# Kernel optimization log

Measured on AMD Instinct MI355X. Metric: run time of the kernel, lower is better.

Reference implementation:

```python
import jax, jax.numpy as jnp
import numpy as np

H_DIM = 64
GRID = 8
NBR = 2.0
BN_EPS = 1e-5
N_SEQ = 64
N_PED = 64
BOTTLENECK = 1024


def setup_inputs() -> dict:
    key = jax.random.key(0)
    k0, k1, k2, k3 = jax.random.split(key, 4)
    batch = N_SEQ * N_PED
    h_states = jax.random.normal(k0, (1, batch, H_DIM), jnp.float32)
    # positions spread over a 4x4 area so some neighbors fall inside the 2.0 neighborhood
    end_pos = jax.random.uniform(k1, (batch, 2), jnp.float32) * 4.0
    rel_pos = jax.random.normal(k2, (batch, 2), jnp.float32)
    starts = jnp.arange(N_SEQ, dtype=jnp.int32) * N_PED
    seq_start_end = jnp.stack([starts, starts + N_PED], axis=1)
    in_dim = GRID * GRID * H_DIM  # 4096
    W = jax.random.normal(k3, (in_dim, BOTTLENECK), jnp.float32) / np.sqrt(in_dim)
    b = jnp.zeros((BOTTLENECK,), jnp.float32)
    gamma = jnp.ones((BOTTLENECK,), jnp.float32)
    beta = jnp.zeros((BOTTLENECK,), jnp.float32)
    return {"h_states": h_states, "seq_start_end": seq_start_end, "end_pos": end_pos,
            "rel_pos": rel_pos, "W": W, "b": b, "gamma": gamma, "beta": beta}


def _pool_scene(hidden, pos):
    # hidden: (n, h), pos: (n, 2). Pair (i, j): ped j binned into ped i's grid.
    n, h = hidden.shape
    g2 = GRID * GRID
    half = NBR / 2.0
    tl_x = pos[:, 0] - half
    tl_y = pos[:, 1] + half
    br_x = pos[:, 0] + half
    br_y = pos[:, 1] - half
    px = pos[None, :, 0]  # (1, n) -> broadcast over i
    py = pos[None, :, 1]
    cell_x = jnp.floor((px - tl_x[:, None]) / NBR * GRID)
    cell_y = jnp.floor((tl_y[:, None] - py) / NBR * GRID)
    grid = (cell_x + cell_y * GRID).astype(jnp.int32) + 1  # slot 0 = trash bin
    oob = ((px >= br_x[:, None]) | (px <= tl_x[:, None]) |
           (py >= tl_y[:, None]) | (py <= br_y[:, None]) |
           jnp.eye(n, dtype=bool))  # self-interaction excluded
    grid = grid + (jnp.arange(n, dtype=jnp.int32) * g2)[:, None]
    grid = jnp.where(oob, 0, grid)  # (n, n)
    src = jnp.broadcast_to(hidden[None], (n, n, h)).reshape(-1, h)
    buf = jnp.zeros((n * g2 + 1, h), hidden.dtype).at[grid.reshape(-1)].add(src)
    return buf[1:].reshape(n, g2 * h)


def reference(h_states, seq_start_end, end_pos, rel_pos, W, b, gamma, beta):
    batch = end_pos.shape[0]
    n_seq = seq_start_end.shape[0]
    n_ped = batch // n_seq  # equal-length scenes by construction
    hid = h_states.reshape(-1, H_DIM).reshape(n_seq, n_ped, H_DIM)
    pos = end_pos.reshape(n_seq, n_ped, 2)
    pool_h = jax.vmap(_pool_scene)(hid, pos).reshape(batch, -1)  # (batch, 4096)
    x = pool_h @ W + b
    # BatchNorm1d in training mode (batch statistics, biased variance)
    mean = jnp.mean(x, axis=0)
    var = jnp.var(x, axis=0)
    x = (x - mean) * jax.lax.rsqrt(var + BN_EPS) * gamma + beta
    return jax.nn.relu(x)
```

## Files before the change

### kernel.cpp

```cpp
#include <hip/hip_runtime.h>
#include <hip/hip_bf16.h>


#define NPED  64
#define BATCH 4096
#define HDIM  64
#define G2    64
#define KDIM  4096
#define NOUT  1024

typedef __attribute__((ext_vector_type(8))) short short8;
typedef __attribute__((ext_vector_type(4))) float f32x4;

__device__ __forceinline__ unsigned short f2bf(float f) {
    __hip_bfloat16 h = __float2bfloat16(f);
    return *reinterpret_cast<unsigned short*>(&h);
}

__device__ __forceinline__ void lds_load16(const void* g, void* l) {
    __builtin_amdgcn_global_load_lds(
        (const __attribute__((address_space(1))) void*)g,
        (__attribute__((address_space(3))) void*)l, 16, 0, 0);
}

__global__ __launch_bounds__(256) void pool_kernel(const float* __restrict__ h,
                                                   const float* __restrict__ pos,
                                                   unsigned short* __restrict__ A2) {
    __shared__ float acc[4][G2 * HDIM];
    __shared__ float pl[NPED * 2];
    int t = threadIdx.x;
    int w = t >> 6, lane = t & 63;
    int p0 = blockIdx.x * 4;
    int sbase = p0 & ~(NPED - 1);
    if (t < 128) pl[t] = pos[sbase * 2 + t];
    #pragma unroll
    for (int c = 0; c < G2; ++c) acc[w][c * HDIM + lane] = 0.f;
    __syncthreads();

    int i = p0 + w;
    int il = i & (NPED - 1);
    float cx0 = pl[2 * il], cy0 = pl[2 * il + 1];
    float tlx = cx0 - 1.f, tly = cy0 + 1.f, brx = cx0 + 1.f, bry = cy0 - 1.f;
    for (int jb = 0; jb < NPED; jb += 8) {
        float hv[8];
        #pragma unroll
        for (int u = 0; u < 8; ++u)
            hv[u] = h[(size_t)(sbase + jb + u) * HDIM + lane];
        #pragma unroll
        for (int u = 0; u < 8; ++u) {
            int j = jb + u;
            float px = pl[2 * j], py = pl[2 * j + 1];
            if (j != il && !(px >= brx || px <= tlx || py >= tly || py <= bry)) {
                int cellx = (int)floorf((px - tlx) * 4.f);
                int celly = (int)floorf((tly - py) * 4.f);
                int cell = cellx + celly * 8;
                if ((unsigned)cell < 64u)
                    atomicAdd(&acc[w][cell * HDIM + lane], hv[u]);
            }
        }
    }
    __syncthreads();

    int mtile = p0 >> 4, r0 = p0 & 15;
    unsigned int* out = (unsigned int*)A2 + (size_t)mtile * 32768 + r0 * 4;
    #pragma unroll
    for (int p = 0; p < 32; ++p) {
        int lin = p * 256 + t;
        int fragidx = lin >> 4;
        int rr = (lin >> 2) & 3, q = lin & 3;
        int k = fragidx * 8 + q * 2;
        unsigned int v = (unsigned int)f2bf(acc[rr][k]) |
                         ((unsigned int)f2bf(acc[rr][k + 1]) << 16);
        out[fragidx * 64 + rr * 4 + q] = v;
    }
}

__global__ __launch_bounds__(256) void wt_kernel(const float* __restrict__ W,
                                                 unsigned short* __restrict__ Wt,
                                                 float* __restrict__ stats) {
    __shared__ unsigned short tile[64][66];
    int k0 = blockIdx.x * 64;
    int n0 = blockIdx.y * 64;
    int t = threadIdx.x;
    if (blockIdx.x == 0 && blockIdx.y < 8) stats[blockIdx.y * 256 + t] = 0.f;
    #pragma unroll
    for (int p = 0; p < 4; ++p) {
        int lin = p * 256 + t;
        int c4 = lin & 15, kl = lin >> 4;
        float4 v = ((const float4*)(W + (size_t)(k0 + kl) * NOUT + n0))[c4];
        tile[c4 * 4 + 0][kl] = f2bf(v.x);
        tile[c4 * 4 + 1][kl] = f2bf(v.y);
        tile[c4 * 4 + 2][kl] = f2bf(v.z);
        tile[c4 * 4 + 3][kl] = f2bf(v.w);
    }
    __syncthreads();
    unsigned int* out = (unsigned int*)Wt;
    #pragma unroll
    for (int p = 0; p < 8; ++p) {
        int lin = p * 256 + t;
        int ku = lin & 31, nl = lin >> 5;
        unsigned int v = (unsigned int)tile[nl][2 * ku] |
                         ((unsigned int)tile[nl][2 * ku + 1] << 16);
        out[(size_t)(n0 + nl) * (KDIM / 2) + (k0 >> 1) + ku] = v;
    }
}

__global__ __launch_bounds__(256, 2) void gemm_kernel(const unsigned short* __restrict__ A2,
                                                      const unsigned short* __restrict__ Bt,
                                                      float* __restrict__ C,
                                                      float* __restrict__ P1,
                                                      float* __restrict__ P2,
                                                      float* __restrict__ P3) {
    __shared__ __align__(16) unsigned short Bs[128 * 64];
    int t = threadIdx.x;
    int w = t >> 6, lane = t & 63;
    int m0 = blockIdx.x * 256, n0 = blockIdx.y * 128;
    int kbase = blockIdx.z * 1024;
    int wm = w * 64;

    f32x4 acc[4][8];
    #pragma unroll
    for (int i = 0; i < 4; ++i)
        #pragma unroll
        for (int j = 0; j < 8; ++j)
            acc[i][j] = (f32x4){0.f, 0.f, 0.f, 0.f};

    int rbase = w * 32 + (lane >> 3);
    int koff = ((lane & 7) ^ (lane >> 3)) * 8;
    const unsigned short* Bg = Bt + (size_t)(n0 + rbase) * KDIM + kbase + koff;
    unsigned short* BsW = Bs + w * 2048 + lane * 8;

    const unsigned short* Abase = A2 + (size_t)((m0 + wm) >> 4) * 65536 + lane * 8;
    int ktile0 = kbase >> 5;

    for (int kt = 0; kt < 1024; kt += 64) {
        #pragma unroll
        for (int q = 0; q < 4; ++q)
            lds_load16(Bg + (size_t)q * 8 * KDIM + kt, BsW + q * 512);
        short8 af[2][4];
        int ktile = ktile0 + (kt >> 5);
        #pragma unroll
        for (int kk = 0; kk < 2; ++kk)
            #pragma unroll
            for (int i = 0; i < 4; ++i)
                af[kk][i] = *(const short8*)(Abase + ((size_t)i * 128 + ktile + kk) * 512);
        __syncthreads();
        #pragma unroll
        for (int kk = 0; kk < 2; ++kk) {
            int chunk = ((kk * 4 + (lane >> 4)) ^ (lane & 7)) * 8;
            #pragma unroll
            for (int j = 0; j < 8; ++j) {
                short8 b = *(const short8*)&Bs[(j * 16 + (lane & 15)) * 64 + chunk];
                #pragma unroll
                for (int i = 0; i < 4; ++i)
                    acc[i][j] = __builtin_amdgcn_mfma_f32_16x16x32_bf16(af[kk][i], b, acc[i][j], 0, 0, 0);
            }
        }
        __syncthreads();
    }

    float* dst = blockIdx.z == 0 ? C : blockIdx.z == 1 ? P1 : blockIdx.z == 2 ? P2 : P3;
    int col0 = n0 + (lane & 15);
    int row0 = m0 + wm + ((lane >> 4) << 2);
    #pragma unroll
    for (int i = 0; i < 4; ++i)
        #pragma unroll
        for (int j = 0; j < 8; ++j)
            #pragma unroll
            for (int r = 0; r < 4; ++r)
                dst[(size_t)(row0 + i * 16 + r) * NOUT + col0 + j * 16] = acc[i][j][r];
}

__global__ __launch_bounds__(256) void combine_stats(float* __restrict__ C,
                                                     const float* __restrict__ P1,
                                                     const float* __restrict__ P2,
                                                     const float* __restrict__ P3,
                                                     float* __restrict__ stats) {
    int t = threadIdx.x;
    int colchunk = blockIdx.x & 3;
    int rowchunk = blockIdx.x >> 2;
    int col = colchunk * 256 + t;
    size_t base = (size_t)rowchunk * 32 * NOUT + col;
    float s = 0.f, s2 = 0.f;
    #pragma unroll 4
    for (int r = 0; r < 32; ++r) {
        size_t ix = base + (size_t)r * NOUT;
        float v = (C[ix] + P1[ix]) + (P2[ix] + P3[ix]);
        C[ix] = v;
        s += v; s2 += v * v;
    }
    atomicAdd(&stats[col], s);
    atomicAdd(&stats[NOUT + col], s2);
}

__global__ __launch_bounds__(256) void norm_kernel(float* __restrict__ C,
                                                   const float* __restrict__ stats,
                                                   const float* __restrict__ gamma,
                                                   const float* __restrict__ beta) {
    int idx = blockIdx.x * 256 + threadIdx.x;
    int col4 = idx & 255;
    float4 x = ((const float4*)C)[idx];
    float4 s = ((const float4*)stats)[col4];
    float4 q = ((const float4*)(stats + NOUT))[col4];
    float4 g = ((const float4*)gamma)[col4];
    float4 b = ((const float4*)beta)[col4];
    const float inv_n = 1.f / 4096.f;
    float m, inv;
    m = s.x * inv_n; inv = rsqrtf(q.x * inv_n - m * m + 1e-5f); x.x = fmaxf((x.x - m) * inv * g.x + b.x, 0.f);
    m = s.y * inv_n; inv = rsqrtf(q.y * inv_n - m * m + 1e-5f); x.y = fmaxf((x.y - m) * inv * g.y + b.y, 0.f);
    m = s.z * inv_n; inv = rsqrtf(q.z * inv_n - m * m + 1e-5f); x.z = fmaxf((x.z - m) * inv * g.z + b.z, 0.f);
    m = s.w * inv_n; inv = rsqrtf(q.w * inv_n - m * m + 1e-5f); x.w = fmaxf((x.w - m) * inv * g.w + b.w, 0.f);
    ((float4*)C)[idx] = x;
}

extern "C" void kernel_launch(void* const* d_in, const int* in_sizes, int n_in,
                              void* d_out, int out_size, void* d_ws, size_t ws_size,
                              hipStream_t stream) {
    const float* h      = (const float*)d_in[0];
    const float* endpos = (const float*)d_in[2];
    const float* W      = (const float*)d_in[4];
    const float* gamma  = (const float*)d_in[6];
    const float* beta   = (const float*)d_in[7];
    float* C = (float*)d_out;

    char* ws = (char*)d_ws;
    size_t off = 0;
    unsigned short* A2 = (unsigned short*)(ws + off); off += (size_t)BATCH * KDIM * 2;
    unsigned short* Wt = (unsigned short*)(ws + off); off += (size_t)NOUT * KDIM * 2;
    float* P1 = (float*)(ws + off); off += (size_t)BATCH * NOUT * 4;
    float* P2 = (float*)(ws + off); off += (size_t)BATCH * NOUT * 4;
    float* P3 = (float*)(ws + off); off += (size_t)BATCH * NOUT * 4;
    float* stats = (float*)(ws + off);

    pool_kernel<<<BATCH / 4, 256, 0, stream>>>(h, endpos, A2);
    wt_kernel<<<dim3(KDIM / 64, NOUT / 64), 256, 0, stream>>>(W, Wt, stats);
    gemm_kernel<<<dim3(BATCH / 256, NOUT / 128, 4), 256, 0, stream>>>(A2, Wt, C, P1, P2, P3);
    combine_stats<<<512, 256, 0, stream>>>(C, P1, P2, P3, stats);
    norm_kernel<<<(BATCH * NOUT / 4) / 256, 256, 0, stream>>>(C, stats, gamma, beta);
}
```

Measured before the change: 174.6 us.

## Replace LDS atomic scatter pooling with ballot-based per-cell gather

The pooling kernel drops the per-wave LDS accumulator and its atomicAdd scatter. Each lane now bins one neighbour, and for each of the 64 cells a wavefront ballot yields the mask of contributing neighbours. Every lane then sums those neighbours' hidden values for its own feature from a scene hidden tile staged in LDS, and writes bf16 straight to the swizzled A layout. Blocks grow to 8 pedestrians and 512 threads. This removes the atomics, the zeroing pass and the second sync, at the cost of 64 ballots per wave and strided 2-byte global stores.

```diff
diff --git a/kernel.cpp b/kernel.cpp
--- a/kernel.cpp
+++ b/kernel.cpp
@@ -23,55 +23,49 @@
         (__attribute__((address_space(3))) void*)l, 16, 0, 0);
 }
 
-__global__ __launch_bounds__(256) void pool_kernel(const float* __restrict__ h,
+__global__ __launch_bounds__(512) void pool_kernel(const float* __restrict__ h,
                                                    const float* __restrict__ pos,
                                                    unsigned short* __restrict__ A2) {
-    __shared__ float acc[4][G2 * HDIM];
+    __shared__ float hs[NPED * HDIM];
     __shared__ float pl[NPED * 2];
     int t = threadIdx.x;
     int w = t >> 6, lane = t & 63;
-    int p0 = blockIdx.x * 4;
+    int p0 = blockIdx.x * 8;
     int sbase = p0 & ~(NPED - 1);
     if (t < 128) pl[t] = pos[sbase * 2 + t];
-    #pragma unroll
-    for (int c = 0; c < G2; ++c) acc[w][c * HDIM + lane] = 0.f;
+    {
+        const float4* src = (const float4*)(h + (size_t)sbase * HDIM);
+        float4* dst = (float4*)hs;
+        dst[t] = src[t];
+        dst[t + 512] = src[t + 512];
+    }
     __syncthreads();
 
     int i = p0 + w;
     int il = i & (NPED - 1);
     float cx0 = pl[2 * il], cy0 = pl[2 * il + 1];
     float tlx = cx0 - 1.f, tly = cy0 + 1.f, brx = cx0 + 1.f, bry = cy0 - 1.f;
-    for (int jb = 0; jb < NPED; jb += 8) {
-        float hv[8];
-        #pragma unroll
-        for (int u = 0; u < 8; ++u)
-            hv[u] = h[(size_t)(sbase + jb + u) * HDIM + lane];
-        #pragma unroll
-        for (int u = 0; u < 8; ++u) {
-            int j = jb + u;
-            float px = pl[2 * j], py = pl[2 * j + 1];
-            if (j != il && !(px >= brx || px <= tlx || py >= tly || py <= bry)) {
-                int cellx = (int)floorf((px - tlx) * 4.f);
-                int celly = (int)floorf((tly - py) * 4.f);
-                int cell = cellx + celly * 8;
-                if ((unsigned)cell < 64u)
-                    atomicAdd(&acc[w][cell * HDIM + lane], hv[u]);
-            }
+    float px = pl[2 * lane], py = pl[2 * lane + 1];
+    bool inb = (lane != il) && !(px >= brx || px <= tlx || py >= tly || py <= bry);
+    int cellx = (int)floorf((px - tlx) * 4.f);
+    int celly = (int)floorf((tly - py) * 4.f);
+    int cell = cellx + celly * 8;
+    inb = inb && ((unsigned)cell < 64u);
+
+    int mtile = i >> 4, r = i & 15;
+    unsigned short* outb = A2 + (size_t)mtile * 65536 + r * 8
+                              + (lane >> 5) * 512 + ((lane >> 3) & 3) * 128 + (lane & 7);
+    const float* hrow = hs + lane;
+    #pragma unroll
+    for (int c = 0; c < 64; ++c) {
+        unsigned long long m = __ballot(inb && (cell == c));
+        float a = 0.f;
+        while (m) {
+            int j = __builtin_ctzll(m);
+            m &= m - 1;
+            a += hrow[j * HDIM];
         }
-    }
-    __syncthreads();
-
-    int mtile = p0 >> 4, r0 = p0 & 15;
-    unsigned int* out = (unsigned int*)A2 + (size_t)mtile * 32768 + r0 * 4;
-    #pragma unroll
-    for (int p = 0; p < 32; ++p) {
-        int lin = p * 256 + t;
-        int fragidx = lin >> 4;
-        int rr = (lin >> 2) & 3, q = lin & 3;
-        int k = fragidx * 8 + q * 2;
-        unsigned int v = (unsigned int)f2bf(acc[rr][k]) |
-                         ((unsigned int)f2bf(acc[rr][k + 1]) << 16);
-        out[fragidx * 64 + rr * 4 + q] = v;
+        outb[c * 1024] = f2bf(a);
     }
 }
 
@@ -232,7 +226,7 @@
     float* P3 = (float*)(ws + off); off += (size_t)BATCH * NOUT * 4;
     float* stats = (float*)(ws + off);
 
-    pool_kernel<<<BATCH / 4, 256, 0, stream>>>(h, endpos, A2);
+    pool_kernel<<<BATCH / 8, 512, 0, stream>>>(h, endpos, A2);
     wt_kernel<<<dim3(KDIM / 64, NOUT / 64), 256, 0, stream>>>(W, Wt, stats);
     gemm_kernel<<<dim3(BATCH / 256, NOUT / 128, 4), 256, 0, stream>>>(A2, Wt, C, P1, P2, P3);
     combine_stats<<<512, 256, 0, stream>>>(C, P1, P2, P3, stats);
```

New measurement: 150.9 us. 1.16x faster.
